# Optimization experiments

Hardware: AMD Instinct MI355X
Metric: run time of the kernel (lower is better)

## Reference

```python
import jax, jax.numpy as jnp
import numpy as np

B, C, L, H, W = 8, 768, 8, 14, 14
HEADS = 12
HD = C // HEADS
SCALE = HD ** (-0.5)
KQ, SQ, PQ = (3, 3, 3), (1, 1, 1), (1, 1, 1)
KKV, SKV, PKV = (3, 3, 3), (1, 2, 2), (1, 1, 1)
EPS = 1e-6


def setup_inputs() -> dict:
    key = jax.random.key(0)
    ks = jax.random.split(key, 16)
    s = 0.02
    inp = {
        'x': jax.random.normal(ks[0], (B, C, L, H, W), jnp.float32),
        'class_token': jax.random.normal(ks[1], (B, C), jnp.float32),
        'Wq': jax.random.normal(ks[2], (C, C), jnp.float32) * s,
        'bq': jnp.zeros((C,), jnp.float32),
        'Wk': jax.random.normal(ks[3], (C, C), jnp.float32) * s,
        'bk': jnp.zeros((C,), jnp.float32),
        'Wv': jax.random.normal(ks[4], (C, C), jnp.float32) * s,
        'bv': jnp.zeros((C,), jnp.float32),
        # depthwise Conv3d kernels: (C, 1, kD, kH, kW), groups=C, no bias
        'conv_q': jax.random.normal(ks[5], (C, 1) + KQ, jnp.float32) * 0.1,
        'conv_k': jax.random.normal(ks[6], (C, 1) + KKV, jnp.float32) * 0.1,
        'conv_v': jax.random.normal(ks[7], (C, 1) + KKV, jnp.float32) * 0.1,
        'lnq_w': jnp.ones((C,), jnp.float32), 'lnq_b': jnp.zeros((C,), jnp.float32),
        'lnk_w': jnp.ones((C,), jnp.float32), 'lnk_b': jnp.zeros((C,), jnp.float32),
        'lnv_w': jnp.ones((C,), jnp.float32), 'lnv_b': jnp.zeros((C,), jnp.float32),
        'Wproj': jax.random.normal(ks[8], (C, C), jnp.float32) * s,
        'bproj': jnp.zeros((C,), jnp.float32),
    }
    return inp


def _linear_keep(x, cls, Wm, b):
    # x: (B,C,l,h,w) -> tokens (B,N,C), prepend cls, linear, split
    Bb, Cc, l, h, w = x.shape
    t = x.reshape(Bb, Cc, -1).transpose(0, 2, 1)          # (B,N,C)
    t = jnp.concatenate([cls[:, None, :], t], axis=1)      # (B,1+N,C)
    y = t @ Wm.T + b
    cls_o = y[:, 0]
    y = y[:, 1:].transpose(0, 2, 1).reshape(Bb, -1, l, h, w)
    return y, cls_o


def _pool(x, wconv, stride, pad, ln_w, ln_b):
    # depthwise 3D conv (groups=C), then LayerNorm over channels
    y = jax.lax.conv_general_dilated(
        x, wconv, window_strides=stride,
        padding=[(p, p) for p in pad],
        dimension_numbers=('NCDHW', 'OIDHW', 'NCDHW'),
        feature_group_count=C)
    y = jnp.moveaxis(y, 1, -1)                            # (B,l,h,w,C)
    mu = y.mean(-1, keepdims=True)
    var = y.var(-1, keepdims=True)
    y = (y - mu) * jax.lax.rsqrt(var + EPS) * ln_w + ln_b
    return jnp.moveaxis(y, -1, 1)


def _to_heads(t):
    # (B,C,l,h,w) -> (B,heads,N,head_dim)
    Bb = t.shape[0]
    return t.reshape(Bb, HEADS, HD, -1).transpose(0, 1, 3, 2)


def _attention(q, k, v, cq, ck, cv, Wp, bp, out_lhw):
    Bb = q.shape[0]
    q = jnp.concatenate([cq.reshape(Bb, HEADS, 1, HD), _to_heads(q)], axis=2)
    k = jnp.concatenate([ck.reshape(Bb, HEADS, 1, HD), _to_heads(k)], axis=2)
    v = jnp.concatenate([cv.reshape(Bb, HEADS, 1, HD), _to_heads(v)], axis=2)
    scores = jnp.einsum('bhqc,bhkc->bhqk', q, k) * SCALE
    attn = jax.nn.softmax(scores, axis=-1)
    o = jnp.einsum('bhqk,bhkc->bhqc', attn, v)            # (B,heads,1+Nq,hd)
    o = o.transpose(0, 2, 1, 3).reshape(Bb, -1, C)        # (B,1+Nq,C)
    o = o @ Wp.T + bp
    cls_o = o[:, 0]
    xo = o[:, 1:].transpose(0, 2, 1).reshape(Bb, C, *out_lhw)
    return xo, cls_o


def reference(x, class_token, Wq, bq, Wk, bk, Wv, bv,
              conv_q, conv_k, conv_v,
              lnq_w, lnq_b, lnk_w, lnk_b, lnv_w, lnv_b,
              Wproj, bproj):
    # pool_first=False: QKV linears first (with cls token), then pooling of the
    # spatial tensors only (cls tokens bypass pooling).
    q, cls_q = _linear_keep(x, class_token, Wq, bq)
    k, cls_k = _linear_keep(x, class_token, Wk, bk)
    v, cls_v = _linear_keep(x, class_token, Wv, bv)
    q = _pool(q, conv_q, SQ, PQ, lnq_w, lnq_b)
    k = _pool(k, conv_k, SKV, PKV, lnk_w, lnk_b)
    v = _pool(v, conv_v, SKV, PKV, lnv_w, lnv_b)
    out_lhw = q.shape[2:]
    return _attention(q, k, v, cls_q, cls_k, cls_v, Wproj, bproj, out_lhw)
```

## Files before the change

### kernel.cpp

```cpp
#include <hip/hip_runtime.h>

#define CDIM 768
#define BATCH 8
#define LDEPTH 8
#define HHEIGHT 14
#define WWIDTH 14
#define NSP 1568
#define NSPX 1576
#define NQTOK 1569
#define NKSP 392
#define NKTOK 393
#define NHEADS 12
#define HEADDIM 64
#define ATTN_SCALE 0.125f
#define LN_EPS 1e-6f
#define MTOK (BATCH * NQTOK)
#define NPAD_X 1792
#define WELEM (CDIM * CDIM)
#define TQP 1792
#define TKP 448

typedef _Float16 f16;
typedef _Float16 f16x8_t __attribute__((ext_vector_type(8)));
typedef _Float16 f16x4_t __attribute__((ext_vector_type(4)));
typedef float f32x4_t __attribute__((ext_vector_type(4)));

__device__ __forceinline__ void gld_lds16(const void* g, void* l) {
  __builtin_amdgcn_global_load_lds(
      (const __attribute__((address_space(1))) void*)g,
      (__attribute__((address_space(3))) void*)l, 16, 0, 0);
}

__global__ __launch_bounds__(256) void convert4_kernel(
    const float* __restrict__ s0, const float* __restrict__ s1,
    const float* __restrict__ s2, const float* __restrict__ s3,
    f16* __restrict__ dst) {
  const int mat = blockIdx.y;
  const float* src = (mat == 0) ? s0 : (mat == 1) ? s1 : (mat == 2) ? s2 : s3;
  int i = (blockIdx.x * 256 + threadIdx.x) * 4;
  if (i < WELEM) {
    float4 v = *(const float4*)&src[i];
    f16x4_t h = {(f16)v.x, (f16)v.y, (f16)v.z, (f16)v.w};
    *(f16x4_t*)&dst[(size_t)mat * WELEM + i] = h;
  }
}

__global__ __launch_bounds__(256) void transpose_x_kernel(
    const float* __restrict__ X, const float* __restrict__ cls,
    f16* __restrict__ Xt) {
  __shared__ float t[32][33];
  const int b = blockIdx.z;
  const int k0 = blockIdx.y * 32;
  const int n0 = blockIdx.x * 32;
  const int tx = threadIdx.x & 31, ty = threadIdx.x >> 5;
#pragma unroll
  for (int i = 0; i < 4; i++) {
    int k = k0 + ty + i * 8;
    int n = n0 + tx;
    float v;
    if (n < NSP)
      v = X[((size_t)b * CDIM + k) * NSP + n];
    else if (n == NSP)
      v = cls[b * CDIM + k];
    else
      v = 0.f;
    t[ty + i * 8][tx] = v;
  }
  __syncthreads();
#pragma unroll
  for (int i = 0; i < 4; i++) {
    int n = n0 + ty + i * 8;
    Xt[((size_t)b * NPAD_X + n) * CDIM + k0 + tx] = (f16)t[tx][ty + i * 8];
  }
}

__global__ __launch_bounds__(256, 2) void gemm_qkv_f16_kernel(
    const f16* __restrict__ W16, const f16* __restrict__ Xt,
    const float* __restrict__ bq, const float* __restrict__ bk,
    const float* __restrict__ bv, f16* __restrict__ OutBase) {
  __shared__ __align__(16) f16 Asm[128 * 32];
  __shared__ __align__(16) f16 Bsm[256 * 32];

  const int bid = blockIdx.x;
  const int b = bid & 7;
  const int rem = bid >> 3;
  const int mat = rem / 42;
  const int rem2 = rem % 42;
  const int m0 = (rem2 / 7) * 128;
  const int n0 = (rem2 % 7) * 256;
  const int tid = threadIdx.x;
  const int lane = tid & 63;
  const int w = tid >> 6;
  const int wr = w >> 1, wc = w & 1;
  const int l15 = lane & 15, l4 = lane >> 4;

  const f16* A16 = W16 + (size_t)mat * WELEM;
  const float* bias = (mat == 0) ? bq : (mat == 1) ? bk : bv;
  f16* Out = OutBase + (size_t)mat * ((size_t)BATCH * CDIM * NSPX);

  const int srow = lane >> 2;
  const int skq = ((lane & 3) ^ ((lane >> 3) & 3)) * 8;
  const f16* Ag = A16 + (size_t)(m0 + w * 32 + srow) * CDIM + skq;
  const f16* Bg = Xt + ((size_t)b * NPAD_X + n0 + w * 64 + srow) * CDIM + skq;
  f16* lA = Asm + w * 32 * 32;
  f16* lB = Bsm + w * 64 * 32;

  const int rsw = (l15 >> 1) & 3;
  const int kchunk = (l4 ^ rsw) * 8;

  f32x4_t acc[4][8];
#pragma unroll
  for (int i = 0; i < 4; i++)
#pragma unroll
    for (int j = 0; j < 8; j++) acc[i][j] = (f32x4_t){0.f, 0.f, 0.f, 0.f};

  for (int k0 = 0; k0 < CDIM; k0 += 32) {
    gld_lds16(Ag + k0, lA);
    gld_lds16(Ag + 16 * CDIM + k0, lA + 16 * 32);
    gld_lds16(Bg + k0, lB);
    gld_lds16(Bg + 16 * CDIM + k0, lB + 16 * 32);
    gld_lds16(Bg + 32 * CDIM + k0, lB + 32 * 32);
    gld_lds16(Bg + 48 * CDIM + k0, lB + 48 * 32);
    __syncthreads();
    f16x8_t af[4];
#pragma unroll
    for (int mi = 0; mi < 4; mi++)
      af[mi] = *(const f16x8_t*)(Asm + (wr * 64 + mi * 16 + l15) * 32 + kchunk);
#pragma unroll
    for (int ni = 0; ni < 8; ni++) {
      f16x8_t bfv =
          *(const f16x8_t*)(Bsm + (wc * 128 + ni * 16 + l15) * 32 + kchunk);
#pragma unroll
      for (int mi = 0; mi < 4; mi++)
        acc[mi][ni] = __builtin_amdgcn_mfma_f32_16x16x32_f16(
            af[mi], bfv, acc[mi][ni], 0, 0, 0);
    }
    __syncthreads();
  }

#pragma unroll
  for (int mi = 0; mi < 4; mi++) {
    const int mbase = m0 + wr * 64 + mi * 16 + l4 * 4;
#pragma unroll
    for (int ni = 0; ni < 8; ni++) {
      const int n = n0 + wc * 128 + ni * 16 + l15;
      if (n < NQTOK) {
#pragma unroll
        for (int r = 0; r < 4; r++) {
          Out[((size_t)b * CDIM + mbase + r) * NSPX + n] =
              (f16)(acc[mi][ni][r] + bias[mbase + r]);
        }
      }
    }
  }
}

__global__ __launch_bounds__(256, 2) void gemm_proj_f16_kernel(
    const f16* __restrict__ Wp16, const f16* __restrict__ o16,
    const float* __restrict__ bias, float* __restrict__ xo,
    float* __restrict__ cls_o) {
  __shared__ __align__(16) f16 Asm[128 * 32];
  __shared__ __align__(16) f16 Bsm[256 * 32];

  const int bid = blockIdx.x;
  const int xcd = bid & 7, pos_ = bid >> 3;
  const int base = (xcd < 4) ? xcd * 38 : 152 + (xcd - 4) * 37;
  const int wgid = base + pos_;
  const int m0 = (wgid / 50) * 128;
  const int n0 = (wgid % 50) * 256;
  const int tid = threadIdx.x;
  const int lane = tid & 63;
  const int w = tid >> 6;
  const int wr = w >> 1, wc = w & 1;
  const int l15 = lane & 15, l4 = lane >> 4;

  const int srow = lane >> 2;
  const int skq = ((lane & 3) ^ ((lane >> 3) & 3)) * 8;
  const f16* Ag = Wp16 + (size_t)(m0 + srow) * CDIM + skq;
  const f16* Bg = o16 + (size_t)(n0 + w * 64 + srow) * CDIM + skq;
  f16* lA = Asm + w * 32 * 32;
  f16* lB = Bsm + w * 64 * 32;
  const f16* Agw = Ag + (size_t)(w * 32) * CDIM;

  const int rsw = (l15 >> 1) & 3;
  const int kchunk = (l4 ^ rsw) * 8;

  f32x4_t acc[4][8];
#pragma unroll
  for (int i = 0; i < 4; i++)
#pragma unroll
    for (int j = 0; j < 8; j++) acc[i][j] = (f32x4_t){0.f, 0.f, 0.f, 0.f};

  for (int k0 = 0; k0 < CDIM; k0 += 32) {
    gld_lds16(Agw + k0, lA);
    gld_lds16(Agw + 16 * CDIM + k0, lA + 16 * 32);
    gld_lds16(Bg + k0, lB);
    gld_lds16(Bg + 16 * CDIM + k0, lB + 16 * 32);
    gld_lds16(Bg + 32 * CDIM + k0, lB + 32 * 32);
    gld_lds16(Bg + 48 * CDIM + k0, lB + 48 * 32);
    __syncthreads();
    f16x8_t af[4];
#pragma unroll
    for (int mi = 0; mi < 4; mi++)
      af[mi] = *(const f16x8_t*)(Asm + (wr * 64 + mi * 16 + l15) * 32 + kchunk);
#pragma unroll
    for (int ni = 0; ni < 8; ni++) {
      f16x8_t bfv =
          *(const f16x8_t*)(Bsm + (wc * 128 + ni * 16 + l15) * 32 + kchunk);
#pragma unroll
      for (int mi = 0; mi < 4; mi++)
        acc[mi][ni] = __builtin_amdgcn_mfma_f32_16x16x32_f16(
            af[mi], bfv, acc[mi][ni], 0, 0, 0);
    }
    __syncthreads();
  }

#pragma unroll
  for (int ni = 0; ni < 8; ni++) {
    const int tok = n0 + wc * 128 + ni * 16 + l15;
    if (tok < MTOK) {
      const int bb = tok / NQTOK;
      const int nn = tok % NQTOK;
#pragma unroll
      for (int mi = 0; mi < 4; mi++) {
        const int mbase = m0 + wr * 64 + mi * 16 + l4 * 4;
#pragma unroll
        for (int r = 0; r < 4; r++) {
          float v = acc[mi][ni][r] + bias[mbase + r];
          if (nn == 0)
            cls_o[bb * CDIM + mbase + r] = v;
          else
            xo[((size_t)bb * CDIM + mbase + r) * (size_t)NSP + nn - 1] = v;
        }
      }
    }
  }
}

__global__ __launch_bounds__(256) void dwconv3_kernel(
    const f16* __restrict__ q_lin, const f16* __restrict__ k_lin,
    const f16* __restrict__ v_lin, const float* __restrict__ cq,
    const float* __restrict__ ck, const float* __restrict__ cv,
    f16* __restrict__ q_pool, f16* __restrict__ k_pool,
    f16* __restrict__ v_pool) {
  __shared__ float xp[10 * 16 * 16];
  __shared__ float wsm[27];
  const int which = blockIdx.y;
  const f16* X = (which == 0) ? k_lin : (which == 1) ? v_lin : q_lin;
  const float* wconv = (which == 0) ? ck : (which == 1) ? cv : cq;
  f16* Out = (which == 0) ? k_pool : (which == 1) ? v_pool : q_pool;
  const int Ho = (which == 2) ? 14 : 7;
  const int s = (which == 2) ? 1 : 2;
  const int c = blockIdx.x % CDIM;
  const int b = blockIdx.x / CDIM;
  const f16* xb = X + ((size_t)b * CDIM + c) * (size_t)NSPX;

  for (int i = threadIdx.x; i < 2560; i += 256) xp[i] = 0.f;
  if (threadIdx.x < 27) wsm[threadIdx.x] = wconv[c * 27 + threadIdx.x];
  __syncthreads();
  for (int i = threadIdx.x; i < NSP; i += 256) {
    int li = i / 196;
    int r = i - li * 196;
    int hi = r / 14;
    int wi = r - hi * 14;
    xp[(li + 1) * 256 + (hi + 1) * 16 + (wi + 1)] = (float)xb[i];
  }
  __syncthreads();

  const int npos = 8 * Ho * Ho;
  const int hh = Ho * Ho;
  f16* ob = Out + ((size_t)b * CDIM + c) * (size_t)npos;
  for (int pos = threadIdx.x; pos < npos; pos += 256) {
    int lo = pos / hh;
    int r = pos - lo * hh;
    int ho = r / Ho;
    int wo = r - ho * Ho;
    const float* bp = &xp[lo * 256 + (ho * s) * 16 + (wo * s)];
    float sum = 0.f;
#pragma unroll
    for (int kd = 0; kd < 3; kd++)
#pragma unroll
      for (int kh = 0; kh < 3; kh++)
#pragma unroll
        for (int kw = 0; kw < 3; kw++)
          sum = fmaf(bp[kd * 256 + kh * 16 + kw], wsm[kd * 9 + kh * 3 + kw],
                     sum);
    ob[pos] = (f16)sum;
  }
}

__global__ __launch_bounds__(256) void ln_pack_qk2_kernel(
    const f16* __restrict__ qp, const f16* __restrict__ kp,
    const float* __restrict__ lnq_w, const float* __restrict__ lnq_b,
    const float* __restrict__ lnk_w, const float* __restrict__ lnk_b,
    f16* __restrict__ Qh, f16* __restrict__ Kh) {
  const int bx = blockIdx.x;
  const bool isq = bx < 49;
  const f16* xp = isq ? qp : kp;
  const float* ln_w = isq ? lnq_w : lnk_w;
  const float* ln_b = isq ? lnq_b : lnk_b;
  f16* OutH = isq ? Qh : Kh;
  const int np = isq ? NSP : NKSP;
  const int tp = isq ? TQP : TKP;
  const int b = blockIdx.y;
  const int p0 = (isq ? bx : bx - 49) * 32;
  const int tid = threadIdx.x;
  const int pl = tid & 31;
  const int grp = tid >> 5;
  const int pos = p0 + pl;
  const bool act = pos < np;
  const f16* Xb = xp + (size_t)b * CDIM * (size_t)np;

  __shared__ __align__(16) f16 tile[32][784];
  __shared__ float r1[8][33], r2[8][33];
  __shared__ float smean[32], srstd[32];

  const int swz = (pl & 7) << 3;
  float s1 = 0.f, s2 = 0.f;
  for (int cc = 0; cc < 12; cc++) {
    const int c0 = grp * 96 + cc * 8;
    f16x8_t hv;
#pragma unroll
    for (int i = 0; i < 8; i++) {
      f16 h = act ? Xb[(size_t)(c0 + i) * np + pos] : (f16)0.f;
      hv[i] = h;
      float v = (float)h;
      s1 += v;
      s2 = fmaf(v, v, s2);
    }
    *(f16x8_t*)&tile[pl][c0 ^ swz] = hv;
  }
  r1[grp][pl] = s1;
  r2[grp][pl] = s2;
  __syncthreads();
  if (tid < 32) {
    float t1 = 0.f, t2 = 0.f;
#pragma unroll
    for (int g = 0; g < 8; g++) { t1 += r1[g][tid]; t2 += r2[g][tid]; }
    float mean = t1 * (1.f / 768.f);
    float var = t2 * (1.f / 768.f) - mean * mean;
    smean[tid] = mean;
    srstd[tid] = rsqrtf(var + LN_EPS);
  }
  __syncthreads();

  const int tl = tid >> 3, d8 = (tid & 7) * 8;
  const float mean = smean[tl], rstd = srstd[tl];
  const bool wv = (p0 + tl) < np;
  const int tswz = (tl & 7) << 3;
#pragma unroll
  for (int h = 0; h < NHEADS; h++) {
    const int c = h * 64 + d8;
    f16x8_t raw = *(const f16x8_t*)&tile[tl][c ^ tswz];
    float4 w1 = *(const float4*)&ln_w[c];
    float4 w2 = *(const float4*)&ln_w[c + 4];
    float4 b1 = *(const float4*)&ln_b[c];
    float4 b2 = *(const float4*)&ln_b[c + 4];
    f16x8_t ov;
    ov[0] = (f16)(((float)raw[0] - mean) * rstd * w1.x + b1.x);
    ov[1] = (f16)(((float)raw[1] - mean) * rstd * w1.y + b1.y);
    ov[2] = (f16)(((float)raw[2] - mean) * rstd * w1.z + b1.z);
    ov[3] = (f16)(((float)raw[3] - mean) * rstd * w1.w + b1.w);
    ov[4] = (f16)(((float)raw[4] - mean) * rstd * w2.x + b2.x);
    ov[5] = (f16)(((float)raw[5] - mean) * rstd * w2.y + b2.y);
    ov[6] = (f16)(((float)raw[6] - mean) * rstd * w2.z + b2.z);
    ov[7] = (f16)(((float)raw[7] - mean) * rstd * w2.w + b2.w);
    if (wv)
      *(uint4*)(OutH +
                (((size_t)(b * NHEADS + h)) * (size_t)tp + (p0 + tl + 1)) * 64 +
                d8) = *(uint4*)&ov;
  }
}

__global__ __launch_bounds__(256) void ln_pack_v_kernel(
    const f16* __restrict__ vp, const f16* __restrict__ vlin,
    const float* __restrict__ ln_w, const float* __restrict__ ln_b,
    f16* __restrict__ Vht) {
  const int b = blockIdx.y;
  const int t0 = blockIdx.x * 32;
  const int tid = threadIdx.x;
  const int pl = tid & 31;
  const int grp = tid >> 5;
  const int t = t0 + pl;
  const int pos = t - 1;
  const bool isv = (t >= 1) && (t < NKTOK);
  const f16* Vb = vp + (size_t)b * CDIM * (size_t)NKSP;

  __shared__ float r1[8][33], r2[8][33];
  __shared__ float smean[32], srstd[32];
  __shared__ __align__(16) f16 vtile[128][40];

  float s1 = 0.f, s2 = 0.f;
  if (isv) {
    for (int c = grp; c < CDIM; c += 8) {
      float v = (float)Vb[(size_t)c * NKSP + pos];
      s1 += v;
      s2 = fmaf(v, v, s2);
    }
  }
  r1[grp][pl] = s1;
  r2[grp][pl] = s2;
  __syncthreads();
  if (tid < 32) {
    float t1 = 0.f, t2 = 0.f;
#pragma unroll
    for (int g = 0; g < 8; g++) { t1 += r1[g][tid]; t2 += r2[g][tid]; }
    float mean = t1 * (1.f / 768.f);
    float var = t2 * (1.f / 768.f) - mean * mean;
    smean[tid] = mean;
    srstd[tid] = rsqrtf(var + LN_EPS);
  }
  __syncthreads();
  const float mean = smean[pl], rstd = srstd[pl];

  for (int cc = 0; cc < 6; cc++) {
#pragma unroll
    for (int i = 0; i < 16; i++) {
      int cl = grp * 16 + i;
      int c = cc * 128 + cl;
      float outv;
      if (isv)
        outv = ((float)Vb[(size_t)c * NKSP + pos] - mean) * rstd * ln_w[c] +
               ln_b[c];
      else if (t == 0)
        outv = (float)vlin[((size_t)b * CDIM + c) * NSPX + NSP];
      else
        outv = 0.f;
      vtile[cl][pl] = (f16)outv;
    }
    __syncthreads();
#pragma unroll
    for (int it = 0; it < 2; it++) {
      int idx = it * 256 + tid;
      int cl = idx >> 2, t8 = (idx & 3) * 8;
      uint4 vv = *(const uint4*)&vtile[cl][t8];
      *(uint4*)(Vht + ((size_t)b * CDIM + cc * 128 + cl) * (size_t)TKP + t0 +
                t8) = vv;
    }
    __syncthreads();
  }
}

__global__ __launch_bounds__(768) void cls_fill_kernel(
    const f16* __restrict__ qlin, const f16* __restrict__ klin,
    f16* __restrict__ Qh, f16* __restrict__ Kh) {
  const int b = blockIdx.x;
  const int c = threadIdx.x;
  Qh[(((size_t)(b * NHEADS + (c >> 6))) * TQP) * 64 + (c & 63)] =
      qlin[((size_t)b * CDIM + c) * NSPX + NSP];
  Kh[(((size_t)(b * NHEADS + (c >> 6))) * TKP) * 64 + (c & 63)] =
      klin[((size_t)b * CDIM + c) * NSPX + NSP];
}

__global__ __launch_bounds__(256) void attn_mfma_kernel(
    const f16* __restrict__ Qh, const f16* __restrict__ Kh,
    const f16* __restrict__ Vht, f16* __restrict__ o16) {
  __shared__ __align__(16) f16 Ks[64 * 72];
  __shared__ __align__(16) f16 Vt[64 * 72];
  const int qt = blockIdx.x, h = blockIdx.y, b = blockIdx.z;
  const int tid = threadIdx.x;
  const int lane = tid & 63;
  const int w = tid >> 6;
  const int l15 = lane & 15, l4 = lane >> 4;
  const int q0 = qt * 256 + w * 64;

  const f16* Qp = Qh + ((size_t)(b * NHEADS + h) * TQP) * 64;
  const f16* Kp = Kh + ((size_t)(b * NHEADS + h) * TKP) * 64;
  const f16* Vp = Vht + ((size_t)(b * NHEADS + h) * 64) * TKP;

  f16x8_t bq[4][2];
#pragma unroll
  for (int qi = 0; qi < 4; qi++)
#pragma unroll
    for (int kf = 0; kf < 2; kf++)
      bq[qi][kf] = *(const f16x8_t*)(Qp + (size_t)(q0 + qi * 16 + l15) * 64 +
                                     kf * 32 + l4 * 8);

  f32x4_t oacc[4][4];
#pragma unroll
  for (int df = 0; df < 4; df++)
#pragma unroll
    for (int qi = 0; qi < 4; qi++) oacc[df][qi] = (f32x4_t){0.f, 0.f, 0.f, 0.f};
  float mrow[4] = {-1e30f, -1e30f, -1e30f, -1e30f};
  float lrow[4] = {0.f, 0.f, 0.f, 0.f};

  const int sr = tid >> 2, sc = (tid & 3) * 16;

  for (int kv0 = 0; kv0 < TKP; kv0 += 64) {
    const f16* kg = Kp + (size_t)(kv0 + sr) * 64 + sc;
    uint4 kl0 = *(const uint4*)kg;
    uint4 kl1 = *(const uint4*)(kg + 8);
    const f16* vg = Vp + (size_t)sr * TKP + kv0 + sc;
    uint4 vl0 = *(const uint4*)vg;
    uint4 vl1 = *(const uint4*)(vg + 8);
    __syncthreads();
    *(uint4*)(Ks + sr * 72 + sc) = kl0;
    *(uint4*)(Ks + sr * 72 + sc + 8) = kl1;
    *(uint4*)(Vt + sr * 72 + sc) = vl0;
    *(uint4*)(Vt + sr * 72 + sc + 8) = vl1;
    __syncthreads();

    f32x4_t sacc[4][4];
#pragma unroll
    for (int ki = 0; ki < 4; ki++)
#pragma unroll
      for (int qi = 0; qi < 4; qi++)
        sacc[ki][qi] = (f32x4_t){0.f, 0.f, 0.f, 0.f};
#pragma unroll
    for (int kf = 0; kf < 2; kf++) {
#pragma unroll
      for (int ki = 0; ki < 4; ki++) {
        f16x8_t ak =
            *(const f16x8_t*)(Ks + (ki * 16 + l15) * 72 + kf * 32 + l4 * 8);
#pragma unroll
        for (int qi = 0; qi < 4; qi++)
          sacc[ki][qi] = __builtin_amdgcn_mfma_f32_16x16x32_f16(
              ak, bq[qi][kf], sacc[ki][qi], 0, 0, 0);
      }
    }

    float pmax[4] = {-1e30f, -1e30f, -1e30f, -1e30f};
#pragma unroll
    for (int ki = 0; ki < 4; ki++) {
      const int keyb = kv0 + ki * 16 + l4 * 4;
#pragma unroll
      for (int qi = 0; qi < 4; qi++) {
#pragma unroll
        for (int rr = 0; rr < 4; rr++) {
          float s = sacc[ki][qi][rr] * ATTN_SCALE;
          if (keyb + rr >= NKTOK) s = -1e30f;
          sacc[ki][qi][rr] = s;
          pmax[qi] = fmaxf(pmax[qi], s);
        }
      }
    }
#pragma unroll
    for (int qi = 0; qi < 4; qi++) {
      pmax[qi] = fmaxf(pmax[qi], __shfl_xor(pmax[qi], 16, 64));
      pmax[qi] = fmaxf(pmax[qi], __shfl_xor(pmax[qi], 32, 64));
      float mnew = fmaxf(mrow[qi], pmax[qi]);
      float alpha = __expf(mrow[qi] - mnew);
      mrow[qi] = mnew;
      lrow[qi] *= alpha;
#pragma unroll
      for (int df = 0; df < 4; df++) {
        oacc[df][qi][0] *= alpha;
        oacc[df][qi][1] *= alpha;
        oacc[df][qi][2] *= alpha;
        oacc[df][qi][3] *= alpha;
      }
    }

#pragma unroll
    for (int ki = 0; ki < 4; ki++) {
      f16x4_t pb[4];
#pragma unroll
      for (int qi = 0; qi < 4; qi++) {
        float p0 = __expf(sacc[ki][qi][0] - mrow[qi]);
        float p1 = __expf(sacc[ki][qi][1] - mrow[qi]);
        float p2 = __expf(sacc[ki][qi][2] - mrow[qi]);
        float p3 = __expf(sacc[ki][qi][3] - mrow[qi]);
        lrow[qi] += p0 + p1 + p2 + p3;
        f16x4_t pv = {(f16)p0, (f16)p1, (f16)p2, (f16)p3};
        pb[qi] = pv;
      }
#pragma unroll
      for (int df = 0; df < 4; df++) {
        f16x4_t av =
            *(const f16x4_t*)(Vt + (df * 16 + l15) * 72 + ki * 16 + l4 * 4);
#pragma unroll
        for (int qi = 0; qi < 4; qi++)
          oacc[df][qi] = __builtin_amdgcn_mfma_f32_16x16x16f16(
              av, pb[qi], oacc[df][qi], 0, 0, 0);
      }
    }
  }

  float inv[4];
#pragma unroll
  for (int qi = 0; qi < 4; qi++) {
    float l = lrow[qi];
    l += __shfl_xor(l, 16, 64);
    l += __shfl_xor(l, 32, 64);
    inv[qi] = 1.f / l;
  }
#pragma unroll
  for (int qi = 0; qi < 4; qi++) {
    const int q = q0 + qi * 16 + l15;
    if (q < NQTOK) {
      f16* op = o16 + ((size_t)(b * NQTOK + q)) * CDIM + h * 64 + l4 * 4;
#pragma unroll
      for (int df = 0; df < 4; df++) {
        f16x4_t ov = {(f16)(oacc[df][qi][0] * inv[qi]),
                      (f16)(oacc[df][qi][1] * inv[qi]),
                      (f16)(oacc[df][qi][2] * inv[qi]),
                      (f16)(oacc[df][qi][3] * inv[qi])};
        *(f16x4_t*)(op + df * 16) = ov;
      }
    }
  }
}

extern "C" void kernel_launch(void* const* d_in, const int* in_sizes, int n_in,
                              void* d_out, int out_size, void* d_ws, size_t ws_size,
                              hipStream_t stream) {
  const float* x      = (const float*)d_in[0];
  const float* cls    = (const float*)d_in[1];
  const float* Wq     = (const float*)d_in[2];
  const float* bq     = (const float*)d_in[3];
  const float* Wk     = (const float*)d_in[4];
  const float* bk     = (const float*)d_in[5];
  const float* Wv     = (const float*)d_in[6];
  const float* bv     = (const float*)d_in[7];
  const float* conv_q = (const float*)d_in[8];
  const float* conv_k = (const float*)d_in[9];
  const float* conv_v = (const float*)d_in[10];
  const float* lnq_w  = (const float*)d_in[11];
  const float* lnq_b  = (const float*)d_in[12];
  const float* lnk_w  = (const float*)d_in[13];
  const float* lnk_b  = (const float*)d_in[14];
  const float* lnv_w  = (const float*)d_in[15];
  const float* lnv_b  = (const float*)d_in[16];
  const float* Wproj  = (const float*)d_in[17];
  const float* bproj  = (const float*)d_in[18];

  char* wsb = (char*)d_ws;
  f16*   Xt     = (f16*)(wsb + 0);
  f16*   W16    = (f16*)(wsb + 22020096);
  f16*   q_lin  = (f16*)(wsb + 26738688);
  f16*   k_lin  = (f16*)(wsb + 46104576);
  f16*   v_lin  = (f16*)(wsb + 65470464);
  f16*   k_pool = (f16*)(wsb + 84836352);
  f16*   v_pool = (f16*)(wsb + 89653248);
  f16*   Kh     = (f16*)(wsb + 94470144);
  f16*   Vht    = (f16*)(wsb + 99975168);
  f16*   q_pool = (f16*)(wsb + 105480192);
  f16*   Qh     = Xt;
  f16*   o16    = v_lin;

  f16* W16p = W16 + (size_t)3 * WELEM;

  convert4_kernel<<<dim3(576, 4), 256, 0, stream>>>(Wq, Wk, Wv, Wproj, W16);

  transpose_x_kernel<<<dim3(56, 24, BATCH), 256, 0, stream>>>(x, cls, Xt);

  gemm_qkv_f16_kernel<<<1008, 256, 0, stream>>>(W16, Xt, bq, bk, bv, q_lin);

  cls_fill_kernel<<<BATCH, 768, 0, stream>>>(q_lin, k_lin, Qh, Kh);

  dwconv3_kernel<<<dim3(BATCH * CDIM, 3), 256, 0, stream>>>(
      q_lin, k_lin, v_lin, conv_q, conv_k, conv_v, q_pool, k_pool, v_pool);

  ln_pack_qk2_kernel<<<dim3(62, BATCH), 256, 0, stream>>>(
      q_pool, k_pool, lnq_w, lnq_b, lnk_w, lnk_b, Qh, Kh);
  ln_pack_v_kernel<<<dim3(14, BATCH), 256, 0, stream>>>(v_pool, v_lin, lnv_w,
                                                        lnv_b, Vht);

  attn_mfma_kernel<<<dim3(7, NHEADS, BATCH), 256, 0, stream>>>(Qh, Kh, Vht,
                                                               o16);

  float* xo = (float*)d_out;
  float* cls_o = (float*)d_out + (size_t)BATCH * CDIM * NSP;
  gemm_proj_f16_kernel<<<300, 256, 0, stream>>>(W16p, o16, bproj, xo, cls_o);
}
```

Before: 364.8 us.

## Split depthwise conv into Q and KV kernels with depth-innermost register reuse

Replaces the single depthwise 3D conv kernel with two kernels. Each stages the padded volume in LDS with depth innermost (w,h,l order), so one thread computes all 8 output depths and reuses loaded values across the kd taps via vector LDS loads. The KV kernel packs 4 channels per block so that 196 threads stay busy on the strided 7x7 outputs, where the old kernel left most threads idle. The cost is larger LDS use per block (about 50KB for KV), which lowers occupancy, and an extra launch.

```diff
diff --git a/kernel.cpp b/kernel.cpp
--- a/kernel.cpp
+++ b/kernel.cpp
@@ -24,6 +24,7 @@
 typedef _Float16 f16x8_t __attribute__((ext_vector_type(8)));
 typedef _Float16 f16x4_t __attribute__((ext_vector_type(4)));
 typedef float f32x4_t __attribute__((ext_vector_type(4)));
+typedef float f32x2_t __attribute__((ext_vector_type(2)));
 
 __device__ __forceinline__ void gld_lds16(const void* g, void* l) {
   __builtin_amdgcn_global_load_lds(
@@ -237,55 +238,129 @@
   }
 }
 
-__global__ __launch_bounds__(256) void dwconv3_kernel(
-    const f16* __restrict__ q_lin, const f16* __restrict__ k_lin,
-    const f16* __restrict__ v_lin, const float* __restrict__ cq,
-    const float* __restrict__ ck, const float* __restrict__ cv,
-    f16* __restrict__ q_pool, f16* __restrict__ k_pool,
-    f16* __restrict__ v_pool) {
-  __shared__ float xp[10 * 16 * 16];
+__global__ __launch_bounds__(256) void dwconv_q_kernel(
+    const f16* __restrict__ q_lin, const float* __restrict__ cq,
+    f16* __restrict__ q_pool) {
+  __shared__ float vol[16 * 196];
   __shared__ float wsm[27];
-  const int which = blockIdx.y;
-  const f16* X = (which == 0) ? k_lin : (which == 1) ? v_lin : q_lin;
-  const float* wconv = (which == 0) ? ck : (which == 1) ? cv : cq;
-  f16* Out = (which == 0) ? k_pool : (which == 1) ? v_pool : q_pool;
-  const int Ho = (which == 2) ? 14 : 7;
-  const int s = (which == 2) ? 1 : 2;
   const int c = blockIdx.x % CDIM;
   const int b = blockIdx.x / CDIM;
-  const f16* xb = X + ((size_t)b * CDIM + c) * (size_t)NSPX;
-
-  for (int i = threadIdx.x; i < 2560; i += 256) xp[i] = 0.f;
-  if (threadIdx.x < 27) wsm[threadIdx.x] = wconv[c * 27 + threadIdx.x];
+  const f16* xb = q_lin + ((size_t)b * CDIM + c) * (size_t)NSPX;
+
+  for (int i = threadIdx.x; i < 16 * 196; i += 256) vol[i] = 0.f;
+  if (threadIdx.x < 27) wsm[threadIdx.x] = cq[c * 27 + threadIdx.x];
   __syncthreads();
   for (int i = threadIdx.x; i < NSP; i += 256) {
     int li = i / 196;
     int r = i - li * 196;
     int hi = r / 14;
     int wi = r - hi * 14;
-    xp[(li + 1) * 256 + (hi + 1) * 16 + (wi + 1)] = (float)xb[i];
-  }
-  __syncthreads();
-
-  const int npos = 8 * Ho * Ho;
-  const int hh = Ho * Ho;
-  f16* ob = Out + ((size_t)b * CDIM + c) * (size_t)npos;
-  for (int pos = threadIdx.x; pos < npos; pos += 256) {
-    int lo = pos / hh;
-    int r = pos - lo * hh;
-    int ho = r / Ho;
-    int wo = r - ho * Ho;
-    const float* bp = &xp[lo * 256 + (ho * s) * 16 + (wo * s)];
-    float sum = 0.f;
-#pragma unroll
-    for (int kd = 0; kd < 3; kd++)
-#pragma unroll
-      for (int kh = 0; kh < 3; kh++)
-#pragma unroll
-        for (int kw = 0; kw < 3; kw++)
-          sum = fmaf(bp[kd * 256 + kh * 16 + kw], wsm[kd * 9 + kh * 3 + kw],
-                     sum);
-    ob[pos] = (f16)sum;
+    vol[(wi + 1) * 196 + (hi + 1) * 12 + (li + 1)] = (float)xb[i];
+  }
+  __syncthreads();
+
+  if (threadIdx.x < 196) {
+    const int ho = threadIdx.x / 14;
+    const int wo = threadIdx.x - ho * 14;
+    float sums[8];
+#pragma unroll
+    for (int lo = 0; lo < 8; lo++) sums[lo] = 0.f;
+#pragma unroll
+    for (int kh = 0; kh < 3; kh++) {
+#pragma unroll
+      for (int kw = 0; kw < 3; kw++) {
+        const float* p = &vol[(wo + kw) * 196 + (ho + kh) * 12];
+        float z[10];
+        *(f32x4_t*)&z[0] = *(const f32x4_t*)p;
+        *(f32x4_t*)&z[4] = *(const f32x4_t*)(p + 4);
+        *(f32x2_t*)&z[8] = *(const f32x2_t*)(p + 8);
+        const float w0 = wsm[0 + kh * 3 + kw];
+        const float w1 = wsm[9 + kh * 3 + kw];
+        const float w2 = wsm[18 + kh * 3 + kw];
+#pragma unroll
+        for (int lo = 0; lo < 8; lo++) {
+          sums[lo] = fmaf(z[lo], w0, sums[lo]);
+          sums[lo] = fmaf(z[lo + 1], w1, sums[lo]);
+          sums[lo] = fmaf(z[lo + 2], w2, sums[lo]);
+        }
+      }
+    }
+    f16* ob = q_pool + ((size_t)b * CDIM + c) * (size_t)NSP;
+    const int hw = ho * 14 + wo;
+#pragma unroll
+    for (int lo = 0; lo < 8; lo++) ob[lo * 196 + hw] = (f16)sums[lo];
+  }
+}
+
+__global__ __launch_bounds__(256) void dwconv_kv_kernel(
+    const f16* __restrict__ k_lin, const f16* __restrict__ v_lin,
+    const float* __restrict__ ck, const float* __restrict__ cv,
+    f16* __restrict__ k_pool, f16* __restrict__ v_pool) {
+  __shared__ float vol4[4][16 * 196];
+  __shared__ float wsm4[4][27];
+  const int which = blockIdx.y;
+  const f16* X = which ? v_lin : k_lin;
+  const float* wconv = which ? cv : ck;
+  f16* Out = which ? v_pool : k_pool;
+  const int cg = blockIdx.x % (CDIM / 4);
+  const int b = blockIdx.x / (CDIM / 4);
+  const int c0 = cg * 4;
+  const f16* xb0 = X + ((size_t)b * CDIM + c0) * (size_t)NSPX;
+
+  for (int i = threadIdx.x; i < 4 * 16 * 196; i += 256)
+    ((float*)vol4)[i] = 0.f;
+  if (threadIdx.x < 108) {
+    int ch = threadIdx.x / 27;
+    int j = threadIdx.x - ch * 27;
+    wsm4[ch][j] = wconv[(c0 + ch) * 27 + j];
+  }
+  __syncthreads();
+  for (int i = threadIdx.x; i < 4 * NSP; i += 256) {
+    int ch = i / NSP;
+    int j = i - ch * NSP;
+    int li = j / 196;
+    int r = j - li * 196;
+    int hi = r / 14;
+    int wi = r - hi * 14;
+    vol4[ch][(wi + 1) * 196 + (hi + 1) * 12 + (li + 1)] =
+        (float)xb0[(size_t)ch * NSPX + j];
+  }
+  __syncthreads();
+
+  if (threadIdx.x < 196) {
+    const int ch = threadIdx.x / 49;
+    const int p2 = threadIdx.x - ch * 49;
+    const int ho = p2 / 7;
+    const int wo = p2 - ho * 7;
+    const float* vol = vol4[ch];
+    const float* wsm = wsm4[ch];
+    float sums[8];
+#pragma unroll
+    for (int lo = 0; lo < 8; lo++) sums[lo] = 0.f;
+#pragma unroll
+    for (int kh = 0; kh < 3; kh++) {
+#pragma unroll
+      for (int kw = 0; kw < 3; kw++) {
+        const float* p = &vol[(wo * 2 + kw) * 196 + (ho * 2 + kh) * 12];
+        float z[10];
+        *(f32x4_t*)&z[0] = *(const f32x4_t*)p;
+        *(f32x4_t*)&z[4] = *(const f32x4_t*)(p + 4);
+        *(f32x2_t*)&z[8] = *(const f32x2_t*)(p + 8);
+        const float w0 = wsm[0 + kh * 3 + kw];
+        const float w1 = wsm[9 + kh * 3 + kw];
+        const float w2 = wsm[18 + kh * 3 + kw];
+#pragma unroll
+        for (int lo = 0; lo < 8; lo++) {
+          sums[lo] = fmaf(z[lo], w0, sums[lo]);
+          sums[lo] = fmaf(z[lo + 1], w1, sums[lo]);
+          sums[lo] = fmaf(z[lo + 2], w2, sums[lo]);
+        }
+      }
+    }
+    f16* ob = Out + ((size_t)b * CDIM + c0 + ch) * (size_t)NKSP;
+    const int hw = ho * 7 + wo;
+#pragma unroll
+    for (int lo = 0; lo < 8; lo++) ob[lo * 49 + hw] = (f16)sums[lo];
   }
 }
 
@@ -648,8 +723,9 @@
 
   cls_fill_kernel<<<BATCH, 768, 0, stream>>>(q_lin, k_lin, Qh, Kh);
 
-  dwconv3_kernel<<<dim3(BATCH * CDIM, 3), 256, 0, stream>>>(
-      q_lin, k_lin, v_lin, conv_q, conv_k, conv_v, q_pool, k_pool, v_pool);
+  dwconv_q_kernel<<<BATCH * CDIM, 256, 0, stream>>>(q_lin, conv_q, q_pool);
+  dwconv_kv_kernel<<<dim3(BATCH * CDIM / 4, 2), 256, 0, stream>>>(
+      k_lin, v_lin, conv_k, conv_v, k_pool, v_pool);
 
   ln_pack_qk2_kernel<<<dim3(62, BATCH), 256, 0, stream>>>(
       q_pool, k_pool, lnq_w, lnq_b, lnk_w, lnk_b, Qh, Kh);
```

Result: faster. 329.7 us (-9.6%).
